# Performance work log

Measured on AMD Instinct MI355X. Metric: run time of the kernel, lower is better.

## Reference

```python
import jax, jax.numpy as jnp
import numpy as np

S, B, IN, OUT = 32, 256, 1024, 1024

def setup_inputs() -> dict:
    key = jax.random.key(0)
    ks = jax.random.split(key, 7)
    return {
        "input": jax.random.normal(ks[0], (S, B, IN), dtype=jnp.float32),
        "weight_mu": jax.random.normal(ks[1], (OUT, IN), dtype=jnp.float32) * 0.1,
        "weight_rho": jax.random.normal(ks[2], (OUT, IN), dtype=jnp.float32) - 3.0,
        "bias_mu": jax.random.normal(ks[3], (OUT,), dtype=jnp.float32) * 0.1,
        "bias_rho": jax.random.normal(ks[4], (OUT,), dtype=jnp.float32) - 3.0,
        "eps_w": jax.random.normal(ks[5], (S, OUT, IN), dtype=jnp.float32),
        "eps_b": jax.random.normal(ks[6], (S, OUT), dtype=jnp.float32),
    }

def reference(input, weight_mu, weight_rho, bias_mu, bias_rho, eps_w, eps_b):
    # sigma = log(1 + exp(rho))  (softplus)
    weight_sigma = jax.nn.softplus(weight_rho)              # (out, in)
    bias_sigma = jax.nn.softplus(bias_rho)                  # (out,)
    # reparameterized samples: (S, out, in) and (S, out)
    weight = weight_mu[None, :, :] + weight_sigma[None, :, :] * eps_w
    bias = bias_mu[None, :] + bias_sigma[None, :] * eps_b
    # batch_linear: per-sample x @ W^T + b
    out = jnp.einsum('sbi,soi->sbo', input, weight) + bias[:, None, :]
    return out
```

## Files before the change

### kernel.cpp

```cpp
#include <hip/hip_runtime.h>
#include <hip/hip_bf16.h>

constexpr int kS   = 32;
constexpr int kB   = 256;
constexpr int kIN  = 1024;
constexpr int kOUT = 1024;

typedef __bf16 v4bf __attribute__((ext_vector_type(4)));
typedef __bf16 v8bf __attribute__((ext_vector_type(8)));
typedef float  v4f  __attribute__((ext_vector_type(4)));

__device__ __forceinline__ float softplus_f(float x) {
    return fmaxf(x, 0.0f) + log1pf(expf(-fabsf(x)));
}

__device__ __forceinline__ v4bf cvt4(float4 v) {
    v4bf r;
    r.x = (__bf16)v.x; r.y = (__bf16)v.y; r.z = (__bf16)v.z; r.w = (__bf16)v.w;
    return r;
}

__global__ void sigma_kernel(const float* __restrict__ rho, float* __restrict__ sigma) {
    int i = blockIdx.x * blockDim.x + threadIdx.x;
    sigma[i] = softplus_f(rho[i]);
}

__global__ void bias_kernel(const float* __restrict__ b_mu, const float* __restrict__ b_rho,
                            const float* __restrict__ eps_b, float* __restrict__ bias_s) {
    int i = blockIdx.x * blockDim.x + threadIdx.x;
    int o = i & (kOUT - 1);
    bias_s[i] = fmaf(softplus_f(b_rho[o]), eps_b[i], b_mu[o]);
}

__global__ __launch_bounds__(256) void dv_main(
        const float* __restrict__ X,
        const float* __restrict__ Wmu,
        const float* __restrict__ Wsig,
        const float* __restrict__ Ew,
        const float* __restrict__ Bs,
        float* __restrict__ O)
{
    constexpr int LS = 40;
    __shared__ __attribute__((aligned(16))) __bf16 Xs[256 * LS];
    __shared__ __attribute__((aligned(16))) __bf16 Ws[64 * LS];

    const int tid    = threadIdx.x;
    const int ot     = blockIdx.x;
    const int s      = blockIdx.y;
    const int o_base = ot * 64;
    const int lane   = tid & 63;
    const int wv     = tid >> 6;
    const int lr     = lane & 15;
    const int kg     = lane >> 4;
    const int m_base = wv * 64;

    const float* Xg = X   + (size_t)s * kB * kIN;
    const float* Eg = Ew  + ((size_t)s * kOUT + o_base) * kIN;
    const float* Mg = Wmu + (size_t)o_base * kIN;
    const float* Sg = Wsig + (size_t)o_base * kIN;

    v4f acc[4][4] = {};

    for (int kk = 0; kk < kIN; kk += 32) {
        #pragma unroll
        for (int j = 0; j < 8; ++j) {
            int f   = j * 256 + tid;
            int row = f >> 3;
            int kq  = f & 7;
            float4 v = *reinterpret_cast<const float4*>(Xg + (size_t)row * kIN + kk + kq * 4);
            *reinterpret_cast<v4bf*>(&Xs[row * LS + kq * 4]) = cvt4(v);
        }
        #pragma unroll
        for (int j = 0; j < 2; ++j) {
            int f   = j * 256 + tid;
            int row = f >> 3;
            int kq  = f & 7;
            size_t idx = (size_t)row * kIN + kk + kq * 4;
            float4 e = *reinterpret_cast<const float4*>(Eg + idx);
            float4 m = *reinterpret_cast<const float4*>(Mg + idx);
            float4 g = *reinterpret_cast<const float4*>(Sg + idx);
            float4 w;
            w.x = fmaf(g.x, e.x, m.x);
            w.y = fmaf(g.y, e.y, m.y);
            w.z = fmaf(g.z, e.z, m.z);
            w.w = fmaf(g.w, e.w, m.w);
            *reinterpret_cast<v4bf*>(&Ws[row * LS + kq * 4]) = cvt4(w);
        }
        __syncthreads();

        v8bf a[4], b[4];
        #pragma unroll
        for (int mf = 0; mf < 4; ++mf)
            a[mf] = *reinterpret_cast<const v8bf*>(&Xs[(m_base + mf * 16 + lr) * LS + kg * 8]);
        #pragma unroll
        for (int nf = 0; nf < 4; ++nf)
            b[nf] = *reinterpret_cast<const v8bf*>(&Ws[(nf * 16 + lr) * LS + kg * 8]);
        #pragma unroll
        for (int mf = 0; mf < 4; ++mf) {
            #pragma unroll
            for (int nf = 0; nf < 4; ++nf)
                acc[mf][nf] = __builtin_amdgcn_mfma_f32_16x16x32_bf16(a[mf], b[nf], acc[mf][nf], 0, 0, 0);
        }
        __syncthreads();
    }

    float bias[4];
    #pragma unroll
    for (int nf = 0; nf < 4; ++nf)
        bias[nf] = Bs[(size_t)s * kOUT + o_base + nf * 16 + lr];

    #pragma unroll
    for (int mf = 0; mf < 4; ++mf) {
        #pragma unroll
        for (int r = 0; r < 4; ++r) {
            int brow = m_base + mf * 16 + kg * 4 + r;
            float* orow = O + ((size_t)s * kB + brow) * kOUT + o_base;
            #pragma unroll
            for (int nf = 0; nf < 4; ++nf)
                orow[nf * 16 + lr] = acc[mf][nf][r] + bias[nf];
        }
    }
}

extern "C" void kernel_launch(void* const* d_in, const int* in_sizes, int n_in,
                              void* d_out, int out_size, void* d_ws, size_t ws_size,
                              hipStream_t stream) {
    const float* input = (const float*)d_in[0];
    const float* w_mu  = (const float*)d_in[1];
    const float* w_rho = (const float*)d_in[2];
    const float* b_mu  = (const float*)d_in[3];
    const float* b_rho = (const float*)d_in[4];
    const float* eps_w = (const float*)d_in[5];
    const float* eps_b = (const float*)d_in[6];
    float* out = (float*)d_out;

    float* sigma  = (float*)d_ws;
    float* bias_s = sigma + (size_t)kOUT * kIN;

    sigma_kernel<<<dim3((kOUT * kIN) / 256), 256, 0, stream>>>(w_rho, sigma);
    bias_kernel<<<dim3((kS * kOUT) / 256), 256, 0, stream>>>(b_mu, b_rho, eps_b, bias_s);

    dim3 grid(kOUT / 64, kS);
    dv_main<<<grid, 256, 0, stream>>>(input, w_mu, sigma, eps_w, bias_s, out);
}
```

Before: 272.2 us.

## Pre-cast input to bf16, shrink output tile, and register-prefetch next K slice

```diff
diff --git a/kernel.cpp b/kernel.cpp
--- a/kernel.cpp
+++ b/kernel.cpp
@@ -5,6 +5,7 @@
 constexpr int kB   = 256;
 constexpr int kIN  = 1024;
 constexpr int kOUT = 1024;
+constexpr int OT   = 32;
 
 typedef __bf16 v4bf __attribute__((ext_vector_type(4)));
 typedef __bf16 v8bf __attribute__((ext_vector_type(8)));
@@ -32,8 +33,19 @@
     bias_s[i] = fmaf(softplus_f(b_rho[o]), eps_b[i], b_mu[o]);
 }
 
-__global__ __launch_bounds__(256) void dv_main(
-        const float* __restrict__ X,
+__global__ void xcast_kernel(const float* __restrict__ X, __bf16* __restrict__ Xb) {
+    size_t i = ((size_t)blockIdx.x * blockDim.x + threadIdx.x) * 8;
+    float4 a = *reinterpret_cast<const float4*>(X + i);
+    float4 b = *reinterpret_cast<const float4*>(X + i + 4);
+    v8bf r;
+    r[0] = (__bf16)a.x; r[1] = (__bf16)a.y; r[2] = (__bf16)a.z; r[3] = (__bf16)a.w;
+    r[4] = (__bf16)b.x; r[5] = (__bf16)b.y; r[6] = (__bf16)b.z; r[7] = (__bf16)b.w;
+    *reinterpret_cast<v8bf*>(Xb + i) = r;
+}
+
+template<bool XBF>
+__global__ __launch_bounds__(256, 4) void dv_main(
+        const void* __restrict__ Xv,
         const float* __restrict__ Wmu,
         const float* __restrict__ Wsig,
         const float* __restrict__ Ew,
@@ -42,71 +54,98 @@
 {
     constexpr int LS = 40;
     __shared__ __attribute__((aligned(16))) __bf16 Xs[256 * LS];
-    __shared__ __attribute__((aligned(16))) __bf16 Ws[64 * LS];
+    __shared__ __attribute__((aligned(16))) __bf16 Ws[OT * LS];
 
     const int tid    = threadIdx.x;
     const int ot     = blockIdx.x;
     const int s      = blockIdx.y;
-    const int o_base = ot * 64;
+    const int o_base = ot * OT;
     const int lane   = tid & 63;
     const int wv     = tid >> 6;
     const int lr     = lane & 15;
     const int kg     = lane >> 4;
     const int m_base = wv * 64;
 
-    const float* Xg = X   + (size_t)s * kB * kIN;
-    const float* Eg = Ew  + ((size_t)s * kOUT + o_base) * kIN;
-    const float* Mg = Wmu + (size_t)o_base * kIN;
+    const float* Eg = Ew   + ((size_t)s * kOUT + o_base) * kIN;
+    const float* Mg = Wmu  + (size_t)o_base * kIN;
     const float* Sg = Wsig + (size_t)o_base * kIN;
+    const int wrow = tid >> 3;
+    const int wkq  = tid & 7;
 
-    v4f acc[4][4] = {};
+    v4f acc[4][2] = {};
+
+    uint4  xr_b[4];
+    float4 xr_f[8];
+    float4 we, wm, wg;
+
+    auto issue = [&](int kk) {
+        if constexpr (XBF) {
+            const __bf16* Xb = (const __bf16*)Xv + (size_t)s * kB * kIN;
+            #pragma unroll
+            for (int j = 0; j < 4; ++j) {
+                int f = j * 256 + tid, row = f >> 2, c = f & 3;
+                xr_b[j] = *reinterpret_cast<const uint4*>(Xb + (size_t)row * kIN + kk + c * 8);
+            }
+        } else {
+            const float* Xg = (const float*)Xv + (size_t)s * kB * kIN;
+            #pragma unroll
+            for (int j = 0; j < 8; ++j) {
+                int f = j * 256 + tid, row = f >> 3, kq = f & 7;
+                xr_f[j] = *reinterpret_cast<const float4*>(Xg + (size_t)row * kIN + kk + kq * 4);
+            }
+        }
+        size_t widx = (size_t)wrow * kIN + kk + wkq * 4;
+        we = *reinterpret_cast<const float4*>(Eg + widx);
+        wm = *reinterpret_cast<const float4*>(Mg + widx);
+        wg = *reinterpret_cast<const float4*>(Sg + widx);
+    };
+
+    issue(0);
 
     for (int kk = 0; kk < kIN; kk += 32) {
-        #pragma unroll
-        for (int j = 0; j < 8; ++j) {
-            int f   = j * 256 + tid;
-            int row = f >> 3;
-            int kq  = f & 7;
-            float4 v = *reinterpret_cast<const float4*>(Xg + (size_t)row * kIN + kk + kq * 4);
-            *reinterpret_cast<v4bf*>(&Xs[row * LS + kq * 4]) = cvt4(v);
+        if constexpr (XBF) {
+            #pragma unroll
+            for (int j = 0; j < 4; ++j) {
+                int f = j * 256 + tid, row = f >> 2, c = f & 3;
+                *reinterpret_cast<uint4*>(&Xs[row * LS + c * 8]) = xr_b[j];
+            }
+        } else {
+            #pragma unroll
+            for (int j = 0; j < 8; ++j) {
+                int f = j * 256 + tid, row = f >> 3, kq = f & 7;
+                *reinterpret_cast<v4bf*>(&Xs[row * LS + kq * 4]) = cvt4(xr_f[j]);
+            }
         }
-        #pragma unroll
-        for (int j = 0; j < 2; ++j) {
-            int f   = j * 256 + tid;
-            int row = f >> 3;
-            int kq  = f & 7;
-            size_t idx = (size_t)row * kIN + kk + kq * 4;
-            float4 e = *reinterpret_cast<const float4*>(Eg + idx);
-            float4 m = *reinterpret_cast<const float4*>(Mg + idx);
-            float4 g = *reinterpret_cast<const float4*>(Sg + idx);
-            float4 w;
-            w.x = fmaf(g.x, e.x, m.x);
-            w.y = fmaf(g.y, e.y, m.y);
-            w.z = fmaf(g.z, e.z, m.z);
-            w.w = fmaf(g.w, e.w, m.w);
-            *reinterpret_cast<v4bf*>(&Ws[row * LS + kq * 4]) = cvt4(w);
-        }
+        float4 w;
+        w.x = fmaf(wg.x, we.x, wm.x);
+        w.y = fmaf(wg.y, we.y, wm.y);
+        w.z = fmaf(wg.z, we.z, wm.z);
+        w.w = fmaf(wg.w, we.w, wm.w);
+        *reinterpret_cast<v4bf*>(&Ws[wrow * LS + wkq * 4]) = cvt4(w);
+
+        if (kk + 32 < kIN) issue(kk + 32);
+
         __syncthreads();
 
-        v8bf a[4], b[4];
+        v8bf a[4], b[2];
         #pragma unroll
         for (int mf = 0; mf < 4; ++mf)
             a[mf] = *reinterpret_cast<const v8bf*>(&Xs[(m_base + mf * 16 + lr) * LS + kg * 8]);
         #pragma unroll
-        for (int nf = 0; nf < 4; ++nf)
+        for (int nf = 0; nf < 2; ++nf)
             b[nf] = *reinterpret_cast<const v8bf*>(&Ws[(nf * 16 + lr) * LS + kg * 8]);
         #pragma unroll
         for (int mf = 0; mf < 4; ++mf) {
             #pragma unroll
-            for (int nf = 0; nf < 4; ++nf)
+            for (int nf = 0; nf < 2; ++nf)
                 acc[mf][nf] = __builtin_amdgcn_mfma_f32_16x16x32_bf16(a[mf], b[nf], acc[mf][nf], 0, 0, 0);
         }
         __syncthreads();
     }
 
-    float bias[4];
+    float bias[2];
     #pragma unroll
-    for (int nf = 0; nf < 4; ++nf)
+    for (int nf = 0; nf < 2; ++nf)
         bias[nf] = Bs[(size_t)s * kOUT + o_base + nf * 16 + lr];
 
     #pragma unroll
@@ -116,7 +155,7 @@
             int brow = m_base + mf * 16 + kg * 4 + r;
             float* orow = O + ((size_t)s * kB + brow) * kOUT + o_base;
             #pragma unroll
-            for (int nf = 0; nf < 4; ++nf)
+            for (int nf = 0; nf < 2; ++nf)
                 orow[nf * 16 + lr] = acc[mf][nf][r] + bias[nf];
         }
     }
@@ -134,12 +173,24 @@
     const float* eps_b = (const float*)d_in[6];
     float* out = (float*)d_out;
 
-    float* sigma  = (float*)d_ws;
-    float* bias_s = sigma + (size_t)kOUT * kIN;
+    const size_t xbf_bytes   = (size_t)kS * kB * kIN * sizeof(__bf16);
+    const size_t sigma_bytes = (size_t)kOUT * kIN * sizeof(float);
+    const size_t bias_bytes  = (size_t)kS * kOUT * sizeof(float);
+    const bool use_xbf = ws_size >= xbf_bytes + sigma_bytes + bias_bytes;
+
+    char* wsb = (char*)d_ws;
+    __bf16* xbf   = (__bf16*)wsb;
+    float*  sigma = use_xbf ? (float*)(wsb + xbf_bytes) : (float*)wsb;
+    float*  bias_s = (float*)((char*)sigma + sigma_bytes);
 
     sigma_kernel<<<dim3((kOUT * kIN) / 256), 256, 0, stream>>>(w_rho, sigma);
     bias_kernel<<<dim3((kS * kOUT) / 256), 256, 0, stream>>>(b_mu, b_rho, eps_b, bias_s);
 
-    dim3 grid(kOUT / 64, kS);
-    dv_main<<<grid, 256, 0, stream>>>(input, w_mu, sigma, eps_w, bias_s, out);
+    dim3 grid(kOUT / OT, kS);
+    if (use_xbf) {
+        xcast_kernel<<<dim3((size_t)kS * kB * kIN / (256 * 8)), 256, 0, stream>>>(input, xbf);
+        dv_main<true><<<grid, 256, 0, stream>>>(xbf, w_mu, sigma, eps_w, bias_s, out);
+    } else {
+        dv_main<false><<<grid, 256, 0, stream>>>(input, w_mu, sigma, eps_w, bias_s, out);
+    }
 }
```

Result: slower. 464.2 us (+70.6%).

## Double-buffer LDS, pack mu/sigma as bf16, precast X, fuse bias

Applied to the files above, without the earlier changes.

```diff
diff --git a/kernel.cpp b/kernel.cpp
--- a/kernel.cpp
+++ b/kernel.cpp
@@ -13,113 +13,182 @@
 __device__ __forceinline__ float softplus_f(float x) {
     return fmaxf(x, 0.0f) + log1pf(expf(-fabsf(x)));
 }
-
-__device__ __forceinline__ v4bf cvt4(float4 v) {
-    v4bf r;
-    r.x = (__bf16)v.x; r.y = (__bf16)v.y; r.z = (__bf16)v.z; r.w = (__bf16)v.w;
-    return r;
-}
-
-__global__ void sigma_kernel(const float* __restrict__ rho, float* __restrict__ sigma) {
-    int i = blockIdx.x * blockDim.x + threadIdx.x;
-    sigma[i] = softplus_f(rho[i]);
-}
-
-__global__ void bias_kernel(const float* __restrict__ b_mu, const float* __restrict__ b_rho,
-                            const float* __restrict__ eps_b, float* __restrict__ bias_s) {
-    int i = blockIdx.x * blockDim.x + threadIdx.x;
-    int o = i & (kOUT - 1);
-    bias_s[i] = fmaf(softplus_f(b_rho[o]), eps_b[i], b_mu[o]);
-}
-
+__device__ __forceinline__ unsigned int bfbits(float x) {
+    __bf16 h = (__bf16)x;
+    unsigned short u;
+    __builtin_memcpy(&u, &h, 2);
+    return (unsigned int)u;
+}
+__device__ __forceinline__ float asf(unsigned int u) {
+    float f; __builtin_memcpy(&f, &u, 4); return f;
+}
+
+__global__ void sigma_pack(const float* __restrict__ mu, const float* __restrict__ rho,
+                           uint4* __restrict__ ms) {
+    int gid = blockIdx.x * blockDim.x + threadIdx.x;
+    float4 m = reinterpret_cast<const float4*>(mu)[gid];
+    float4 r = reinterpret_cast<const float4*>(rho)[gid];
+    uint4 o;
+    o.x = bfbits(m.x) | (bfbits(softplus_f(r.x)) << 16);
+    o.y = bfbits(m.y) | (bfbits(softplus_f(r.y)) << 16);
+    o.z = bfbits(m.z) | (bfbits(softplus_f(r.z)) << 16);
+    o.w = bfbits(m.w) | (bfbits(softplus_f(r.w)) << 16);
+    ms[gid] = o;
+}
+
+__global__ void xcast_kernel(const float* __restrict__ X, __bf16* __restrict__ Xb) {
+    size_t i = ((size_t)blockIdx.x * blockDim.x + threadIdx.x) * 8;
+    float4 a = *reinterpret_cast<const float4*>(X + i);
+    float4 b = *reinterpret_cast<const float4*>(X + i + 4);
+    v8bf r;
+    r[0] = (__bf16)a.x; r[1] = (__bf16)a.y; r[2] = (__bf16)a.z; r[3] = (__bf16)a.w;
+    r[4] = (__bf16)b.x; r[5] = (__bf16)b.y; r[6] = (__bf16)b.z; r[7] = (__bf16)b.w;
+    *reinterpret_cast<v8bf*>(Xb + i) = r;
+}
+
+template<bool XBF>
 __global__ __launch_bounds__(256) void dv_main(
-        const float* __restrict__ X,
-        const float* __restrict__ Wmu,
-        const float* __restrict__ Wsig,
+        const void* __restrict__ Xv,
+        const unsigned int* __restrict__ MS,
         const float* __restrict__ Ew,
-        const float* __restrict__ Bs,
+        const float* __restrict__ Bmu,
+        const float* __restrict__ Brho,
+        const float* __restrict__ Eb,
         float* __restrict__ O)
 {
     constexpr int LS = 40;
-    __shared__ __attribute__((aligned(16))) __bf16 Xs[256 * LS];
-    __shared__ __attribute__((aligned(16))) __bf16 Ws[64 * LS];
-
-    const int tid    = threadIdx.x;
-    const int ot     = blockIdx.x;
-    const int s      = blockIdx.y;
+    __shared__ __attribute__((aligned(16))) __bf16 Xs[2][128 * LS];
+    __shared__ __attribute__((aligned(16))) __bf16 Ws[2][64 * LS];
+
+    const int tid = threadIdx.x;
+    const int bb  = blockIdx.x;
+    const int rr_ = bb & 15, gg = bb >> 4;
+    const int pid = gg * 8 + (rr_ & 7);
+    const int mt  = rr_ >> 3;
+    const int s   = pid >> 4;
+    const int ot  = pid & 15;
     const int o_base = ot * 64;
-    const int lane   = tid & 63;
-    const int wv     = tid >> 6;
-    const int lr     = lane & 15;
-    const int kg     = lane >> 4;
-    const int m_base = wv * 64;
-
-    const float* Xg = X   + (size_t)s * kB * kIN;
-    const float* Eg = Ew  + ((size_t)s * kOUT + o_base) * kIN;
-    const float* Mg = Wmu + (size_t)o_base * kIN;
-    const float* Sg = Wsig + (size_t)o_base * kIN;
-
-    v4f acc[4][4] = {};
-
-    for (int kk = 0; kk < kIN; kk += 32) {
+    const int m_glob = mt * 128;
+
+    const int lane = tid & 63, wv = tid >> 6;
+    const int lr = lane & 15, kg = lane >> 4;
+
+    const int wrow0 = tid >> 3;
+    const int wc    = tid & 7;
+    const float*        Eg  = Ew + ((size_t)s * kOUT + o_base) * kIN;
+    const unsigned int* MSg = MS + (size_t)o_base * kIN;
+
+    v4f acc[2][4] = {};
+
+    uint4  xr[2];
+    float4 xf[4];
+    float4 er[2];
+    uint4  pr[2];
+
+#define STAGE_ISSUE(KK)                                                          \
+    {                                                                            \
+        if constexpr (XBF) {                                                     \
+            const __bf16* Xb = (const __bf16*)Xv + ((size_t)s * kB + m_glob) * kIN; \
+            _Pragma("unroll")                                                    \
+            for (int j = 0; j < 2; ++j) {                                        \
+                int slot = j * 256 + tid, row = slot >> 2, c = slot & 3;         \
+                xr[j] = *reinterpret_cast<const uint4*>(Xb + (size_t)row * kIN + (KK) + c * 8); \
+            }                                                                    \
+        } else {                                                                 \
+            const float* Xg = (const float*)Xv + ((size_t)s * kB + m_glob) * kIN; \
+            _Pragma("unroll")                                                    \
+            for (int j = 0; j < 4; ++j) {                                        \
+                int slot = j * 256 + tid, row = slot >> 3, c = slot & 7;         \
+                xf[j] = *reinterpret_cast<const float4*>(Xg + (size_t)row * kIN + (KK) + c * 4); \
+            }                                                                    \
+        }                                                                        \
+        _Pragma("unroll")                                                        \
+        for (int j = 0; j < 2; ++j) {                                            \
+            int row = j * 32 + wrow0;                                            \
+            er[j] = *reinterpret_cast<const float4*>(Eg + (size_t)row * kIN + (KK) + wc * 4); \
+            pr[j] = *reinterpret_cast<const uint4*>(MSg + (size_t)row * kIN + (KK) + wc * 4); \
+        }                                                                        \
+    }
+
+#define STAGE_STORE(P)                                                           \
+    {                                                                            \
+        if constexpr (XBF) {                                                     \
+            _Pragma("unroll")                                                    \
+            for (int j = 0; j < 2; ++j) {                                        \
+                int slot = j * 256 + tid, row = slot >> 2, c = slot & 3;         \
+                *reinterpret_cast<uint4*>(&Xs[P][row * LS + c * 8]) = xr[j];     \
+            }                                                                    \
+        } else {                                                                 \
+            _Pragma("unroll")                                                    \
+            for (int j = 0; j < 4; ++j) {                                        \
+                int slot = j * 256 + tid, row = slot >> 3, c = slot & 7;         \
+                v4bf w;                                                          \
+                w[0] = (__bf16)xf[j].x; w[1] = (__bf16)xf[j].y;                  \
+                w[2] = (__bf16)xf[j].z; w[3] = (__bf16)xf[j].w;                  \
+                *reinterpret_cast<v4bf*>(&Xs[P][row * LS + c * 4]) = w;          \
+            }                                                                    \
+        }                                                                        \
+        _Pragma("unroll")                                                        \
+        for (int j = 0; j < 2; ++j) {                                            \
+            int row = j * 32 + wrow0;                                            \
+            v4bf w;                                                              \
+            unsigned int p0 = pr[j].x, p1 = pr[j].y, p2 = pr[j].z, p3 = pr[j].w; \
+            w[0] = (__bf16)fmaf(asf(p0 & 0xffff0000u), er[j].x, asf(p0 << 16));  \
+            w[1] = (__bf16)fmaf(asf(p1 & 0xffff0000u), er[j].y, asf(p1 << 16));  \
+            w[2] = (__bf16)fmaf(asf(p2 & 0xffff0000u), er[j].z, asf(p2 << 16));  \
+            w[3] = (__bf16)fmaf(asf(p3 & 0xffff0000u), er[j].w, asf(p3 << 16));  \
+            *reinterpret_cast<v4bf*>(&Ws[P][row * LS + wc * 4]) = w;             \
+        }                                                                        \
+    }
+
+#define COMPUTE(P)                                                               \
+    {                                                                            \
+        v8bf a[2], bfr[4];                                                       \
+        _Pragma("unroll")                                                        \
+        for (int mf = 0; mf < 2; ++mf)                                           \
+            a[mf] = *reinterpret_cast<const v8bf*>(&Xs[P][(wv * 32 + mf * 16 + lr) * LS + kg * 8]); \
+        _Pragma("unroll")                                                        \
+        for (int nf = 0; nf < 4; ++nf)                                           \
+            bfr[nf] = *reinterpret_cast<const v8bf*>(&Ws[P][(nf * 16 + lr) * LS + kg * 8]); \
+        _Pragma("unroll")                                                        \
+        for (int mf = 0; mf < 2; ++mf)                                           \
+            _Pragma("unroll")                                                    \
+            for (int nf = 0; nf < 4; ++nf)                                       \
+                acc[mf][nf] = __builtin_amdgcn_mfma_f32_16x16x32_bf16(a[mf], bfr[nf], acc[mf][nf], 0, 0, 0); \
+    }
+
+    STAGE_ISSUE(0);
+    for (int kk = 0; kk < kIN; kk += 64) {
+        STAGE_STORE(0);
+        STAGE_ISSUE(kk + 32);
+        __syncthreads();
+        COMPUTE(0);
+        STAGE_STORE(1);
+        if (kk + 64 < kIN) STAGE_ISSUE(kk + 64);
+        __syncthreads();
+        COMPUTE(1);
+    }
+
+    float bias[4];
+    #pragma unroll
+    for (int nf = 0; nf < 4; ++nf) {
+        int o = o_base + nf * 16 + lr;
+        bias[nf] = fmaf(softplus_f(Brho[o]), Eb[(size_t)s * kOUT + o], Bmu[o]);
+    }
+    #pragma unroll
+    for (int mf = 0; mf < 2; ++mf) {
         #pragma unroll
-        for (int j = 0; j < 8; ++j) {
-            int f   = j * 256 + tid;
-            int row = f >> 3;
-            int kq  = f & 7;
-            float4 v = *reinterpret_cast<const float4*>(Xg + (size_t)row * kIN + kk + kq * 4);
-            *reinterpret_cast<v4bf*>(&Xs[row * LS + kq * 4]) = cvt4(v);
-        }
-        #pragma unroll
-        for (int j = 0; j < 2; ++j) {
-            int f   = j * 256 + tid;
-            int row = f >> 3;
-            int kq  = f & 7;
-            size_t idx = (size_t)row * kIN + kk + kq * 4;
-            float4 e = *reinterpret_cast<const float4*>(Eg + idx);
-            float4 m = *reinterpret_cast<const float4*>(Mg + idx);
-            float4 g = *reinterpret_cast<const float4*>(Sg + idx);
-            float4 w;
-            w.x = fmaf(g.x, e.x, m.x);
-            w.y = fmaf(g.y, e.y, m.y);
-            w.z = fmaf(g.z, e.z, m.z);
-            w.w = fmaf(g.w, e.w, m.w);
-            *reinterpret_cast<v4bf*>(&Ws[row * LS + kq * 4]) = cvt4(w);
-        }
-        __syncthreads();
-
-        v8bf a[4], b[4];
-        #pragma unroll
-        for (int mf = 0; mf < 4; ++mf)
-            a[mf] = *reinterpret_cast<const v8bf*>(&Xs[(m_base + mf * 16 + lr) * LS + kg * 8]);
-        #pragma unroll
-        for (int nf = 0; nf < 4; ++nf)
-            b[nf] = *reinterpret_cast<const v8bf*>(&Ws[(nf * 16 + lr) * LS + kg * 8]);
-        #pragma unroll
-        for (int mf = 0; mf < 4; ++mf) {
+        for (int rr = 0; rr < 4; ++rr) {
+            int mrow = m_glob + wv * 32 + mf * 16 + kg * 4 + rr;
+            float* orow = O + ((size_t)s * kB + mrow) * kOUT + o_base;
             #pragma unroll
             for (int nf = 0; nf < 4; ++nf)
-                acc[mf][nf] = __builtin_amdgcn_mfma_f32_16x16x32_bf16(a[mf], b[nf], acc[mf][nf], 0, 0, 0);
+                orow[nf * 16 + lr] = acc[mf][nf][rr] + bias[nf];
         }
-        __syncthreads();
-    }
-
-    float bias[4];
-    #pragma unroll
-    for (int nf = 0; nf < 4; ++nf)
-        bias[nf] = Bs[(size_t)s * kOUT + o_base + nf * 16 + lr];
-
-    #pragma unroll
-    for (int mf = 0; mf < 4; ++mf) {
-        #pragma unroll
-        for (int r = 0; r < 4; ++r) {
-            int brow = m_base + mf * 16 + kg * 4 + r;
-            float* orow = O + ((size_t)s * kB + brow) * kOUT + o_base;
-            #pragma unroll
-            for (int nf = 0; nf < 4; ++nf)
-                orow[nf * 16 + lr] = acc[mf][nf][r] + bias[nf];
-        }
-    }
+    }
+#undef STAGE_ISSUE
+#undef STAGE_STORE
+#undef COMPUTE
 }
 
 extern "C" void kernel_launch(void* const* d_in, const int* in_sizes, int n_in,
@@ -134,12 +203,20 @@
     const float* eps_b = (const float*)d_in[6];
     float* out = (float*)d_out;
 
-    float* sigma  = (float*)d_ws;
-    float* bias_s = sigma + (size_t)kOUT * kIN;
-
-    sigma_kernel<<<dim3((kOUT * kIN) / 256), 256, 0, stream>>>(w_rho, sigma);
-    bias_kernel<<<dim3((kS * kOUT) / 256), 256, 0, stream>>>(b_mu, b_rho, eps_b, bias_s);
-
-    dim3 grid(kOUT / 64, kS);
-    dv_main<<<grid, 256, 0, stream>>>(input, w_mu, sigma, eps_w, bias_s, out);
-}
+    const size_t ms_bytes  = (size_t)kOUT * kIN * 4;
+    const size_t xbf_bytes = (size_t)kS * kB * kIN * sizeof(__bf16);
+    const bool use_xbf = ws_size >= ms_bytes + xbf_bytes;
+
+    unsigned int* ms = (unsigned int*)d_ws;
+    __bf16* xbf = (__bf16*)((char*)d_ws + ms_bytes);
+
+    sigma_pack<<<dim3((kOUT * kIN) / (256 * 4)), 256, 0, stream>>>(w_mu, w_rho, (uint4*)ms);
+
+    dim3 grid(2 * 16 * kS);
+    if (use_xbf) {
+        xcast_kernel<<<dim3((size_t)kS * kB * kIN / (256 * 8)), 256, 0, stream>>>(input, xbf);
+        dv_main<true><<<grid, 256, 0, stream>>>(xbf, ms, eps_w, b_mu, b_rho, eps_b, out);
+    } else {
+        dv_main<false><<<grid, 256, 0, stream>>>(input, ms, eps_w, b_mu, b_rho, eps_b, out);
+    }
+}
```

Result: slower. 335.5 us (+23.3%).
